# Kernel tuning notes

Measured on AMD Instinct MI355X. Metric: run time of the kernel, lower is better.

Reference implementation:

```python
import jax, jax.numpy as jnp
import numpy as np

T, B, N = 1000, 64, 512
DT = 0.01
EL, VR, TR, TINF = -0.07, -0.07, -0.06, -0.05
A_VAL = 2.6239240169525146
A1_VAL = -0.015625353902578354
A2_VAL = -1.0590057373046875
B_VAL = 12.77495288848877
G_VAL = 45.24007797241211
K1, K2 = 200.0, 20.0
R1, R2 = 0.3858567178249359, -1.1421641111373901
C = 1.0


def setup_inputs() -> dict:
    key = jax.random.key(0)
    x = jax.random.normal(key, (T, B, N), dtype=jnp.float32)
    linear = jnp.ones((1, N), jnp.float32)
    a = jnp.full((1, N), A_VAL, jnp.float32)
    A1 = jnp.full((1, N), A1_VAL * C, jnp.float32)
    A2 = jnp.full((1, N), A2_VAL * C, jnp.float32)
    return {"x": x, "linear": linear, "a": a, "A1": A1, "A2": A2}


def _spike(v):
    # Heaviside step (forward of SurrGradSpike)
    return (v > 0).astype(v.dtype)


def reference(x, linear, a, A1, A2):
    G = G_VAL * C

    def step(state, xt):
        V, i1, i2, Thr = state
        i1 = i1 - K1 * i1 * DT
        i2 = i2 - K2 * i2 * DT
        V = V + DT * (linear * xt + i1 + i2 - G * (V - EL)) / C
        Thr = Thr + DT * (a * (V - EL) - B_VAL * (Thr - TINF))
        spk = _spike(V - Thr)
        i1 = (1.0 - spk) * i1 + spk * (R1 * i1 + A1)
        i2 = (1.0 - spk) * i2 + spk * (R2 * i2 + A2)
        Thr = (1.0 - spk) * Thr + spk * jnp.maximum(Thr, TR)
        V = (1.0 - spk) * V + spk * VR
        return (V, i1, i2, Thr), spk

    Bd, Nd = x.shape[1], x.shape[2]
    init = (
        jnp.full((Bd, Nd), EL, x.dtype),   # V
        jnp.zeros((Bd, Nd), x.dtype),      # i1
        jnp.zeros((Bd, Nd), x.dtype),      # i2
        jnp.full((Bd, Nd), TINF, x.dtype), # Thr
    )
    _, spikes = jax.lax.scan(step, init, x)
    return spikes  # [T, B, N] (original returns np.array of per-step spikes)
```

## Files before the change

### kernel.cpp

```cpp
#include <hip/hip_runtime.h>


#define T_STEPS 1000
#define B_DIM 64
#define N_DIM 512
#define BN (B_DIM * N_DIM)

#define K_CHUNK 20
#define NCHUNK (T_STEPS / K_CHUNK)

#define C_DT   0.01f
#define C_EL   (-0.07f)
#define C_VR   (-0.07f)
#define C_TR   (-0.06f)
#define C_TINF (-0.05f)
#define C_B    12.77495288848877f
#define C_G    45.24007797241211f
#define C_K1   200.0f
#define C_K2   20.0f
#define C_R1   0.3858567178249359f
#define C_R2   (-1.1421641111373901f)

typedef const __attribute__((address_space(1))) void* gp_t;
typedef __attribute__((address_space(3))) void* lp_t;
typedef __attribute__((address_space(3))) float* lpf_t;

__device__ __forceinline__ float mn_step(float xt, float lin, float av,
                                         float A1v, float A2v,
                                         float& V, float& i1, float& i2,
                                         float& Thr)
{
#pragma clang fp contract(off)
    i1 = i1 - (C_K1 * i1) * C_DT;
    i2 = i2 - (C_K2 * i2) * C_DT;
    float p  = lin * xt;
    float q  = p + i1;
    float r  = q + i2;
    float e  = V - C_EL;
    float g  = C_G * e;
    float s  = r - g;
    float d  = C_DT * s;
    V = V + d;
    float e2 = V - C_EL;
    float u  = av * e2;
    float w  = Thr - C_TINF;
    float bw = C_B * w;
    float s2 = u - bw;
    float d2 = C_DT * s2;
    Thr = Thr + d2;
    float diff = V - Thr;
    bool  sb   = diff > 0.0f;
    float spk  = sb ? 1.0f : 0.0f;
    float i1r = (C_R1 * i1) + A1v;
    float i2r = (C_R2 * i2) + A2v;
    i1  = sb ? i1r : i1;
    i2  = sb ? i2r : i2;
    float tm = fmaxf(Thr, C_TR);
    Thr = sb ? tm : Thr;
    V   = sb ? C_VR : V;
    return spk;
}

__global__ __launch_bounds__(128) void mn_neuron_kernel(
    const float* __restrict__ x, const float* __restrict__ linear,
    const float* __restrict__ a, const float* __restrict__ A1,
    const float* __restrict__ A2, float* __restrict__ out)
{
#pragma clang fp contract(off)
    __shared__ float lds[2][K_CHUNK][64];

    const int lane = threadIdx.x & 63;
    const int wid  = threadIdx.x >> 6;
    const int blk  = blockIdx.x;

    if (wid == 1) {
        const float* pl = x + (size_t)(lane >> 4) * BN
                            + (size_t)blk * 64 + (size_t)(lane & 15) * 4;

        {
#pragma unroll
            for (int s = 0; s < K_CHUNK / 4; ++s) {
                __builtin_amdgcn_global_load_lds(
                    (gp_t)(pl + (size_t)(s * 4) * BN),
                    (lp_t)&lds[0][s * 4][0], 16, 0, 0);
            }
            __builtin_amdgcn_s_waitcnt(0x0F70);
        }
        __builtin_amdgcn_s_barrier();

        for (int c = 0; c < NCHUNK; ++c) {
            if (c + 1 < NCHUNK) {
                const float* pc = pl + (size_t)((c + 1) * K_CHUNK) * BN;
                float* dst = &lds[(c + 1) & 1][0][0];
#pragma unroll
                for (int s = 0; s < K_CHUNK / 4; ++s) {
                    __builtin_amdgcn_global_load_lds(
                        (gp_t)(pc + (size_t)(s * 4) * BN),
                        (lp_t)(dst + s * 4 * 64), 16, 0, 0);
                }
                __builtin_amdgcn_s_waitcnt(0x0F70);
            }
            __builtin_amdgcn_s_barrier();
        }
    } else {
        const int idx = blk * 64 + lane;
        const int n   = idx & (N_DIM - 1);

        const float lin = linear[n];
        const float av  = a[n];
        const float A1v = A1[n];
        const float A2v = A2[n];

        float V   = C_EL;
        float i1  = 0.0f;
        float i2  = 0.0f;
        float Thr = C_TINF;

        float* op = out + idx;

        __builtin_amdgcn_s_barrier();

        for (int c = 0; c < NCHUNK; ++c) {
            lpf_t lptr = (lpf_t)&lds[c & 1][0][lane];

            float xv[K_CHUNK];
            asm volatile(
                "ds_read_b32 %0,  %20 offset:0\n\t"
                "ds_read_b32 %1,  %20 offset:256\n\t"
                "ds_read_b32 %2,  %20 offset:512\n\t"
                "ds_read_b32 %3,  %20 offset:768\n\t"
                "ds_read_b32 %4,  %20 offset:1024\n\t"
                "ds_read_b32 %5,  %20 offset:1280\n\t"
                "ds_read_b32 %6,  %20 offset:1536\n\t"
                "ds_read_b32 %7,  %20 offset:1792\n\t"
                "ds_read_b32 %8,  %20 offset:2048\n\t"
                "ds_read_b32 %9,  %20 offset:2304\n\t"
                "ds_read_b32 %10, %20 offset:2560\n\t"
                "ds_read_b32 %11, %20 offset:2816\n\t"
                "ds_read_b32 %12, %20 offset:3072\n\t"
                "ds_read_b32 %13, %20 offset:3328\n\t"
                "ds_read_b32 %14, %20 offset:3584\n\t"
                "ds_read_b32 %15, %20 offset:3840\n\t"
                "ds_read_b32 %16, %20 offset:4096\n\t"
                "ds_read_b32 %17, %20 offset:4352\n\t"
                "ds_read_b32 %18, %20 offset:4608\n\t"
                "ds_read_b32 %19, %20 offset:4864\n\t"
                "s_waitcnt lgkmcnt(0)"
                : "=&v"(xv[0]),  "=&v"(xv[1]),  "=&v"(xv[2]),  "=&v"(xv[3]),
                  "=&v"(xv[4]),  "=&v"(xv[5]),  "=&v"(xv[6]),  "=&v"(xv[7]),
                  "=&v"(xv[8]),  "=&v"(xv[9]),  "=&v"(xv[10]), "=&v"(xv[11]),
                  "=&v"(xv[12]), "=&v"(xv[13]), "=&v"(xv[14]), "=&v"(xv[15]),
                  "=&v"(xv[16]), "=&v"(xv[17]), "=&v"(xv[18]), "=&v"(xv[19])
                : "v"(lptr));

            __builtin_amdgcn_s_barrier();

#pragma unroll
            for (int j = 0; j < K_CHUNK; ++j) {
                float spk = mn_step(xv[j], lin, av, A1v, A2v, V, i1, i2, Thr);
                __builtin_nontemporal_store(spk, op);
                op += BN;
            }
        }
    }
}

extern "C" void kernel_launch(void* const* d_in, const int* in_sizes, int n_in,
                              void* d_out, int out_size, void* d_ws, size_t ws_size,
                              hipStream_t stream) {
    const float* x      = (const float*)d_in[0];
    const float* linear = (const float*)d_in[1];
    const float* a      = (const float*)d_in[2];
    const float* A1     = (const float*)d_in[3];
    const float* A2     = (const float*)d_in[4];
    float* out = (float*)d_out;

    mn_neuron_kernel<<<BN / 64, 128, 0, stream>>>(x, linear, a, A1, A2, out);
}
```

Baseline: 240.5 us.

## Deepen async global-to-LDS prefetch ring from double buffer to eight buffers

The loader wave now keeps up to seven chunks of input in flight using an eight-slot LDS ring, instead of prefetching only one chunk ahead. Each wait is a partial vmcnt wait rather than waiting for all loads, and a tail of decreasing vmcnt waits with barriers keeps the barrier count matched to the compute wave. The aim is to hide global-memory latency in this latency-bound scan. In exchange, LDS use per block grows about fourfold, which could limit how many blocks fit on a CU.

```diff
diff --git a/kernel.cpp b/kernel.cpp
--- a/kernel.cpp
+++ b/kernel.cpp
@@ -8,6 +8,7 @@
 
 #define K_CHUNK 20
 #define NCHUNK (T_STEPS / K_CHUNK)
+#define NBUF 8
 
 #define C_DT   0.01f
 #define C_EL   (-0.07f)
@@ -67,7 +68,7 @@
     const float* __restrict__ A2, float* __restrict__ out)
 {
 #pragma clang fp contract(off)
-    __shared__ float lds[2][K_CHUNK][64];
+    __shared__ float lds[NBUF][K_CHUNK][64];
 
     const int lane = threadIdx.x & 63;
     const int wid  = threadIdx.x >> 6;
@@ -77,31 +78,39 @@
         const float* pl = x + (size_t)(lane >> 4) * BN
                             + (size_t)blk * 64 + (size_t)(lane & 15) * 4;
 
-        {
+        auto issue_chunk = [&](int ch) {
+            const float* pc = pl + (size_t)(ch * K_CHUNK) * BN;
+            float* dst = &lds[ch & (NBUF - 1)][0][0];
 #pragma unroll
             for (int s = 0; s < K_CHUNK / 4; ++s) {
                 __builtin_amdgcn_global_load_lds(
-                    (gp_t)(pl + (size_t)(s * 4) * BN),
-                    (lp_t)&lds[0][s * 4][0], 16, 0, 0);
+                    (gp_t)(pc + (size_t)(s * 4) * BN),
+                    (lp_t)(dst + s * 4 * 64), 16, 0, 0);
             }
-            __builtin_amdgcn_s_waitcnt(0x0F70);
-        }
+        };
+
+        for (int ch = 0; ch < NBUF - 1; ++ch) issue_chunk(ch);
+        asm volatile("s_waitcnt vmcnt(30)" ::: "memory");
         __builtin_amdgcn_s_barrier();
 
-        for (int c = 0; c < NCHUNK; ++c) {
-            if (c + 1 < NCHUNK) {
-                const float* pc = pl + (size_t)((c + 1) * K_CHUNK) * BN;
-                float* dst = &lds[(c + 1) & 1][0][0];
-#pragma unroll
-                for (int s = 0; s < K_CHUNK / 4; ++s) {
-                    __builtin_amdgcn_global_load_lds(
-                        (gp_t)(pc + (size_t)(s * 4) * BN),
-                        (lp_t)(dst + s * 4 * 64), 16, 0, 0);
-                }
-                __builtin_amdgcn_s_waitcnt(0x0F70);
-            }
+        for (int c = 0; c <= NCHUNK - NBUF; ++c) {
+            issue_chunk(c + NBUF - 1);
+            asm volatile("s_waitcnt vmcnt(30)" ::: "memory");
             __builtin_amdgcn_s_barrier();
         }
+        asm volatile("s_waitcnt vmcnt(25)" ::: "memory");
+        __builtin_amdgcn_s_barrier();
+        asm volatile("s_waitcnt vmcnt(20)" ::: "memory");
+        __builtin_amdgcn_s_barrier();
+        asm volatile("s_waitcnt vmcnt(15)" ::: "memory");
+        __builtin_amdgcn_s_barrier();
+        asm volatile("s_waitcnt vmcnt(10)" ::: "memory");
+        __builtin_amdgcn_s_barrier();
+        asm volatile("s_waitcnt vmcnt(5)" ::: "memory");
+        __builtin_amdgcn_s_barrier();
+        asm volatile("s_waitcnt vmcnt(0)" ::: "memory");
+        __builtin_amdgcn_s_barrier();
+        __builtin_amdgcn_s_barrier();
     } else {
         const int idx = blk * 64 + lane;
         const int n   = idx & (N_DIM - 1);
@@ -121,7 +130,7 @@
         __builtin_amdgcn_s_barrier();
 
         for (int c = 0; c < NCHUNK; ++c) {
-            lpf_t lptr = (lpf_t)&lds[c & 1][0][lane];
+            lpf_t lptr = (lpf_t)&lds[c & (NBUF - 1)][0][lane];
 
             float xv[K_CHUNK];
             asm volatile(
```

After: 246.1 us. +2.3%, slower.
